# Performance work log

Hardware: AMD Instinct MI355X
Metric: run time of the kernel (lower is better)

The kernel has to match this reference:

```python
import jax, jax.numpy as jnp
import numpy as np

PARTIAL_DATA_THRESHOLD = 0.1  # threshold on squared NN distance (ChamferDistance returns squared dists)


def setup_inputs() -> dict:
    key = jax.random.key(0)
    k1, k2 = jax.random.split(key)
    scan_vertices = jax.random.normal(k1, (50000, 3), dtype=jnp.float32)      # N x 3
    template_vertices = jax.random.normal(k2, (6890, 3), dtype=jnp.float32)   # M x 3
    return {"scan_vertices": scan_vertices, "template_vertices": template_vertices}


def reference(scan_vertices, template_vertices):
    # Directional (template -> scan) Chamfer: for each template point, squared
    # distance to nearest scan point; then sum distances below threshold.
    # d2[m, n] = |t_m|^2 + |s_n|^2 - 2 t_m . s_n
    t_sq = jnp.sum(template_vertices * template_vertices, axis=-1)            # [M]
    s_sq = jnp.sum(scan_vertices * scan_vertices, axis=-1)                    # [N]
    cross = jnp.einsum('md,nd->mn', template_vertices, scan_vertices)         # [M, N]
    d2 = t_sq[:, None] + s_sq[None, :] - 2.0 * cross                          # [M, N]
    template2scan = jnp.min(d2, axis=1)                                       # [M]
    mask = template2scan < PARTIAL_DATA_THRESHOLD
    return jnp.sum(jnp.where(mask, template2scan, 0.0))
```

## Files before the change

kernel.cpp:

```cpp
#include <hip/hip_runtime.h>
#include <hip/hip_bf16.h>

#define BLK 256
#define WPB 4
#define TB 4
#define TSPLITS 54
#define SA 10
#define SGROUPS 40
#define COLS (TSPLITS * TB * 32)
#define THRESH 0.1f
#define KEY_MAX 0xFFFFFFFFu
#define ONE2 0x3F803F80u

typedef __attribute__((ext_vector_type(8))) short short8;
typedef __attribute__((ext_vector_type(16))) float floatx16;

__device__ __forceinline__ unsigned short f2bf(float x) {
    unsigned u = __float_as_uint(x);
    unsigned r = u + 0x7FFFu + ((u >> 16) & 1u);
    return (unsigned short)(r >> 16);
}
__device__ __forceinline__ float bf2f(unsigned short h) {
    return __uint_as_float(((unsigned)h) << 16);
}
__device__ __forceinline__ unsigned packsplit(float v) {
    const unsigned short h = f2bf(v);
    const unsigned short l = f2bf(v - bf2f(h));
    return (unsigned)h | ((unsigned)l << 16);
}

__device__ __forceinline__ unsigned f2key(float f) {
    unsigned b = __float_as_uint(f);
    return (b & 0x80000000u) ? ~b : (b | 0x80000000u);
}
__device__ __forceinline__ float key2f(unsigned k) {
    return __uint_as_float((k & 0x80000000u) ? (k & 0x7FFFFFFFu) : ~k);
}

__device__ __forceinline__ uint4 build_scan_frag(float x, float y, float z, bool hi) {
    const float s2 = fmaf(x, x, fmaf(y, y, z * z));
    const float c0 = -2.0f * (hi ? z : x);
    const float c1 = hi ? s2 : (-2.0f * y);
    const unsigned w01 = packsplit(c0);
    const unsigned w23 = packsplit(c1);
    uint4 u;
    u.x = w01; u.y = w01;
    u.z = hi ? ONE2 : w23;
    u.w = w23;
    return u;
}

__device__ __forceinline__ uint4 build_tmpl_frag(const float* __restrict__ tmpl,
                                                 int c, bool hi) {
    const float x = tmpl[3 * c + 0], y = tmpl[3 * c + 1], z = tmpl[3 * c + 2];
    const float t2 = fmaf(x, x, fmaf(y, y, z * z));
    const float a0 = hi ? z : x;
    const float a1 = hi ? t2 : y;
    const unsigned short h0 = f2bf(a0);
    const unsigned short l0 = f2bf(a0 - bf2f(h0));
    const unsigned short h1 = f2bf(a1);
    const unsigned short l1 = f2bf(a1 - bf2f(h1));
    uint4 u;
    u.x = (unsigned)h0 | ((unsigned)h0 << 16);
    u.y = (unsigned)l0 | ((unsigned)l0 << 16);
    u.z = hi ? ((unsigned)h1 | ((unsigned)l1 << 16))
             : ((unsigned)h1 | ((unsigned)h1 << 16));
    u.w = hi ? ONE2
             : ((unsigned)l1 | ((unsigned)l1 << 16));
    return u;
}

__device__ __forceinline__ float dtile_min(const floatx16 d, float mn) {
    const float t0 = fminf(fminf(d[0], d[1]), d[2]);
    const float t1 = fminf(fminf(d[3], d[4]), d[5]);
    const float t2 = fminf(fminf(d[6], d[7]), d[8]);
    const float t3 = fminf(fminf(d[9], d[10]), d[11]);
    const float t4 = fminf(fminf(d[12], d[13]), d[14]);
    const float u0 = fminf(fminf(t0, t1), t2);
    const float u1 = fminf(fminf(t3, t4), d[15]);
    return fminf(fminf(u0, u1), mn);
}

__global__ __launch_bounds__(BLK, 4) void pdl_main(const float* __restrict__ scan,
                                                   const float* __restrict__ tmpl,
                                                   unsigned* __restrict__ partial,
                                                   float* __restrict__ out,
                                                   int N, int M) {
    const int tid = threadIdx.x;
    const int wave = tid >> 6, lane = tid & 63;
    const bool hi = (lane >= 32);
    const int tsplit = blockIdx.x;
    const int sgroup = blockIdx.y;
    const int ssplit = sgroup * WPB + wave;

    if (tsplit == 0 && sgroup == 0 && tid == 0) out[0] = 0.0f;

    __shared__ unsigned lmin[TB * 32];
    if (tid < TB * 32) lmin[tid] = KEY_MAX;

    union U { uint4 u; short8 s; };

    U B[TB];
    const int cbase = tsplit * (TB * 32) + (lane & 31);
#pragma unroll
    for (int j = 0; j < TB; ++j) {
        int c = cbase + j * 32;
        if (c > M - 1) c = M - 1;
        B[j].u = build_tmpl_frag(tmpl, c, hi);
    }

    float mn[TB];
#pragma unroll
    for (int j = 0; j < TB; ++j) mn[j] = 3e30f;

    floatx16 zacc;
#pragma unroll
    for (int r = 0; r < 16; ++r) zacc[r] = 0.0f;

    const int nbase = ssplit * (SA * 32) + (lane & 31);
    int n0 = nbase; if (n0 > N - 1) n0 = N - 1;
    float x = scan[3 * n0 + 0], y = scan[3 * n0 + 1], z = scan[3 * n0 + 2];
#pragma unroll 1
    for (int f = 0; f < SA; ++f) {
        int n1 = nbase + (f + 1) * 32; if (n1 > N - 1) n1 = N - 1;
        const float nx = scan[3 * n1 + 0];
        const float ny = scan[3 * n1 + 1];
        const float nz = scan[3 * n1 + 2];
        U a; a.u = build_scan_frag(x, y, z, hi);
        {
            const floatx16 d0 =
                __builtin_amdgcn_mfma_f32_32x32x16_bf16(a.s, B[0].s, zacc, 0, 0, 0);
            const floatx16 d1 =
                __builtin_amdgcn_mfma_f32_32x32x16_bf16(a.s, B[1].s, zacc, 0, 0, 0);
            mn[0] = dtile_min(d0, mn[0]);
            mn[1] = dtile_min(d1, mn[1]);
        }
        {
            const floatx16 d0 =
                __builtin_amdgcn_mfma_f32_32x32x16_bf16(a.s, B[2].s, zacc, 0, 0, 0);
            const floatx16 d1 =
                __builtin_amdgcn_mfma_f32_32x32x16_bf16(a.s, B[3].s, zacc, 0, 0, 0);
            mn[2] = dtile_min(d0, mn[2]);
            mn[3] = dtile_min(d1, mn[3]);
        }
        x = nx; y = ny; z = nz;
    }

    __syncthreads();

#pragma unroll
    for (int j = 0; j < TB; ++j) {
        const float o = __shfl_xor(mn[j], 32, 64);
        const float v = fminf(mn[j], o);
        if (lane < 32) atomicMin(&lmin[j * 32 + lane], f2key(v));
    }
    __syncthreads();

    const size_t base = (size_t)sgroup * COLS + (size_t)tsplit * (TB * 32);
    if (tid < TB * 32) partial[base + tid] = lmin[tid];
}

__global__ __launch_bounds__(BLK) void pdl_final(const unsigned* __restrict__ partial,
                                                 float* __restrict__ out, int M) {
    const int m = blockIdx.x * BLK + threadIdx.x;
    float s = 0.0f;
    if (m < M) {
        unsigned k = KEY_MAX;
#pragma unroll 4
        for (int g = 0; g < SGROUPS; ++g)
            k = min(k, partial[(size_t)g * COLS + m]);
        const float v = key2f(k);
        if (v < THRESH) s = v;
    }
#pragma unroll
    for (int off = 32; off > 0; off >>= 1) s += __shfl_down(s, off, 64);

    __shared__ float ls[BLK / 64];
    const int lane = threadIdx.x & 63;
    const int w = threadIdx.x >> 6;
    if (lane == 0) ls[w] = s;
    __syncthreads();
    if (threadIdx.x == 0) {
        float t = 0.0f;
#pragma unroll
        for (int i = 0; i < BLK / 64; ++i) t += ls[i];
        atomicAdd(out, t);
    }
}

extern "C" void kernel_launch(void* const* d_in, const int* in_sizes, int n_in,
                              void* d_out, int out_size, void* d_ws, size_t ws_size,
                              hipStream_t stream) {
    const float* scan = (const float*)d_in[0];
    const float* tmpl = (const float*)d_in[1];
    float* out = (float*)d_out;

    const int N = in_sizes[0] / 3;
    const int M = in_sizes[1] / 3;

    unsigned* partial = (unsigned*)d_ws;

    dim3 grid(TSPLITS, SGROUPS);
    pdl_main<<<grid, BLK, 0, stream>>>(scan, tmpl, partial, out, N, M);

    pdl_final<<<(M + BLK - 1) / BLK, BLK, 0, stream>>>(partial, out, M);
}
```

Measured before the change: 73.82 us.

## Fuse final reduction into main kernel via last-block ticket and rebalance scan split

Removes the separate final-reduction kernel. Each block now takes a ticket from an atomic counter (cleared by a memset), and the last block to finish does the column-min over scan groups plus the thresholded sum. The scan split is rebalanced to fewer groups (18) with more fragments per wave (22), which cuts the partial buffer traffic and the final reduction's work. The cost is a memset launch, a threadfence per block, and a serial tail reduction done by a single block.

```diff
diff --git a/kernel.cpp b/kernel.cpp
--- a/kernel.cpp
+++ b/kernel.cpp
@@ -5,9 +5,11 @@
 #define WPB 4
 #define TB 4
 #define TSPLITS 54
-#define SA 10
-#define SGROUPS 40
+#define SGROUPS 18
+#define SA 22
 #define COLS (TSPLITS * TB * 32)
+#define NBLOCKS (TSPLITS * SGROUPS)
+#define CTR_OFF 524288
 #define THRESH 0.1f
 #define KEY_MAX 0xFFFFFFFFu
 #define ONE2 0x3F803F80u
@@ -35,19 +37,6 @@
 }
 __device__ __forceinline__ float key2f(unsigned k) {
     return __uint_as_float((k & 0x80000000u) ? (k & 0x7FFFFFFFu) : ~k);
-}
-
-__device__ __forceinline__ uint4 build_scan_frag(float x, float y, float z, bool hi) {
-    const float s2 = fmaf(x, x, fmaf(y, y, z * z));
-    const float c0 = -2.0f * (hi ? z : x);
-    const float c1 = hi ? s2 : (-2.0f * y);
-    const unsigned w01 = packsplit(c0);
-    const unsigned w23 = packsplit(c1);
-    uint4 u;
-    u.x = w01; u.y = w01;
-    u.z = hi ? ONE2 : w23;
-    u.w = w23;
-    return u;
 }
 
 __device__ __forceinline__ uint4 build_tmpl_frag(const float* __restrict__ tmpl,
@@ -84,6 +73,7 @@
 __global__ __launch_bounds__(BLK, 4) void pdl_main(const float* __restrict__ scan,
                                                    const float* __restrict__ tmpl,
                                                    unsigned* __restrict__ partial,
+                                                   unsigned* __restrict__ ctr,
                                                    float* __restrict__ out,
                                                    int N, int M) {
     const int tid = threadIdx.x;
@@ -92,8 +82,6 @@
     const int tsplit = blockIdx.x;
     const int sgroup = blockIdx.y;
     const int ssplit = sgroup * WPB + wave;
-
-    if (tsplit == 0 && sgroup == 0 && tid == 0) out[0] = 0.0f;
 
     __shared__ unsigned lmin[TB * 32];
     if (tid < TB * 32) lmin[tid] = KEY_MAX;
@@ -126,7 +114,14 @@
         const float nx = scan[3 * n1 + 0];
         const float ny = scan[3 * n1 + 1];
         const float nz = scan[3 * n1 + 2];
-        U a; a.u = build_scan_frag(x, y, z, hi);
+        const float s2 = fmaf(x, x, fmaf(y, y, z * z));
+        const float c0 = -2.0f * (hi ? z : x);
+        const float c1 = hi ? s2 : (-2.0f * y);
+        U a;
+        a.u.x = packsplit(c0);
+        a.u.y = a.u.x;
+        a.u.z = hi ? ONE2 : packsplit(c1);
+        a.u.w = hi ? packsplit(c1) : a.u.z;
         {
             const floatx16 d0 =
                 __builtin_amdgcn_mfma_f32_32x32x16_bf16(a.s, B[0].s, zacc, 0, 0, 0);
@@ -158,33 +153,37 @@
 
     const size_t base = (size_t)sgroup * COLS + (size_t)tsplit * (TB * 32);
     if (tid < TB * 32) partial[base + tid] = lmin[tid];
-}
-
-__global__ __launch_bounds__(BLK) void pdl_final(const unsigned* __restrict__ partial,
-                                                 float* __restrict__ out, int M) {
-    const int m = blockIdx.x * BLK + threadIdx.x;
+
+    __threadfence();
+    __syncthreads();
+    __shared__ unsigned tkt;
+    if (tid == 0) tkt = atomicAdd(ctr, 1u);
+    __syncthreads();
+    if (tkt != NBLOCKS - 1) return;
+
+    __threadfence();
     float s = 0.0f;
-    if (m < M) {
-        unsigned k = KEY_MAX;
-#pragma unroll 4
-        for (int g = 0; g < SGROUPS; ++g)
+#pragma unroll 1
+    for (int c = 0; c < COLS / BLK; ++c) {
+        const int m = c * BLK + tid;
+        unsigned k = partial[m];
+#pragma unroll
+        for (int g = 1; g < SGROUPS; ++g)
             k = min(k, partial[(size_t)g * COLS + m]);
         const float v = key2f(k);
-        if (v < THRESH) s = v;
+        if (m < M && v < THRESH) s += v;
     }
 #pragma unroll
     for (int off = 32; off > 0; off >>= 1) s += __shfl_down(s, off, 64);
 
     __shared__ float ls[BLK / 64];
-    const int lane = threadIdx.x & 63;
-    const int w = threadIdx.x >> 6;
-    if (lane == 0) ls[w] = s;
-    __syncthreads();
-    if (threadIdx.x == 0) {
+    if (lane == 0) ls[wave] = s;
+    __syncthreads();
+    if (tid == 0) {
         float t = 0.0f;
 #pragma unroll
         for (int i = 0; i < BLK / 64; ++i) t += ls[i];
-        atomicAdd(out, t);
+        out[0] = t;
     }
 }
 
@@ -199,9 +198,10 @@
     const int M = in_sizes[1] / 3;
 
     unsigned* partial = (unsigned*)d_ws;
+    unsigned* ctr = (unsigned*)((char*)d_ws + CTR_OFF);
+
+    hipMemsetAsync(ctr, 0, 4, stream);
 
     dim3 grid(TSPLITS, SGROUPS);
-    pdl_main<<<grid, BLK, 0, stream>>>(scan, tmpl, partial, out, N, M);
-
-    pdl_final<<<(M + BLK - 1) / BLK, BLK, 0, stream>>>(partial, out, M);
-}
+    pdl_main<<<grid, BLK, 0, stream>>>(scan, tmpl, partial, ctr, out, N, M);
+}
```

After: 145.0 us. 96.5% more time.
